# Kernel optimization log

Hardware: AMD Instinct MI355X
Metric: run time of the kernel (lower is better)

The kernel has to match this reference:

```python
import jax, jax.numpy as jnp
import numpy as np

S = 60            # voxel grid side
N = 100000        # active voxels
M_PAD = 60000     # padded pairs per kernel offset
C_IN = 64
C_OUT = 64
KV = 27           # kernel volume (3^3)
CENTER = 13


def _build_maps():
    rng = np.random.default_rng(0)
    lin = rng.choice(S ** 3, size=N, replace=False)
    coords = np.stack(np.unravel_index(lin, (S, S, S)), axis=1).astype(np.int64)  # [N,3]
    lut = -np.ones(S ** 3, dtype=np.int64)
    lut[lin] = np.arange(N)
    imap = -np.ones((KV - 1, M_PAD), dtype=np.int32)
    omap = -np.ones((KV - 1, M_PAD), dtype=np.int32)
    row = 0
    for k in range(KV):
        if k == CENTER:
            continue
        d = np.array([k // 9 - 1, (k // 3) % 3 - 1, k % 3 - 1])
        nb = coords + d
        valid = np.all((nb >= 0) & (nb < S), axis=1)
        linnb = nb[:, 0] * S * S + nb[:, 1] * S + nb[:, 2]
        j = np.where(valid, lut[np.clip(linnb, 0, S ** 3 - 1)], -1)
        mask = j >= 0
        src = np.nonzero(mask)[0].astype(np.int32)   # input idx (gather)
        dst = j[mask].astype(np.int32)               # output idx (scatter)
        m = min(src.shape[0], M_PAD)
        imap[row, :m] = src[:m]
        omap[row, :m] = dst[:m]
        row += 1
    return imap, omap


def setup_inputs() -> dict:
    key = jax.random.key(0)
    kf, kw = jax.random.split(key)
    feats = jax.random.normal(kf, (N, C_IN), dtype=jnp.float32)
    stdv = 1.0 / np.sqrt(C_OUT * KV)
    kernel = jax.random.uniform(kw, (KV, C_IN, C_OUT), dtype=jnp.float32,
                                minval=-stdv, maxval=stdv)
    imap_np, omap_np = _build_maps()
    return {
        "feats": feats,
        "kernel": kernel,
        "imap": jnp.asarray(imap_np),
        "omap": jnp.asarray(omap_np),
    }


def reference(feats, kernel, imap, omap):
    # Submanifold sparse 3D conv: center weight applied densely,
    # 26 neighbor offsets via gather -> per-offset GEMM -> scatter-add.
    # feats: [N, Cin], kernel: [27, Cin, Cout], imap/omap: [26, M] (-1 = pad)
    koff = jnp.concatenate([jnp.arange(CENTER), jnp.arange(CENTER + 1, KV)])
    w_off = kernel[koff]                                   # [26, Cin, Cout]
    out = feats @ kernel[CENTER]                           # [N, Cout] center GEMM
    valid = (imap >= 0)                                    # [26, M]
    gathered = feats[jnp.clip(imap, 0)] * valid[..., None].astype(feats.dtype)  # [26, M, Cin]
    partial = jnp.einsum('kmc,kco->kmo', gathered, w_off)  # [26, M, Cout]
    dst = jnp.where(valid, omap, 0).reshape(-1)            # padded rows contribute zeros
    out = out.at[dst].add(partial.reshape(-1, partial.shape[-1]))
    return out
```

## Files before the change

kernel.cpp:

```cpp
#include <hip/hip_runtime.h>


#define N_PTS 100000
#define MPAD  60000
#define C     64
#define NSL   27

typedef short bf16x8 __attribute__((ext_vector_type(8)));
typedef float f32x4  __attribute__((ext_vector_type(4)));

static __device__ inline unsigned short f2bf(float x) {
    unsigned int u = __float_as_uint(x);
    u += 0x7fffu + ((u >> 16) & 1u);
    return (unsigned short)(u >> 16);
}

#define FEATS16_BYTES ((size_t)(N_PTS + 1) * C * 2)
#define WFRAG_OFF     (((FEATS16_BYTES) + 255) & ~(size_t)255)
#define WFRAG_BYTES   ((size_t)NSL * 8192)
#define NBR_OFF       (WFRAG_OFF + WFRAG_BYTES)
#define NBR_BYTES     ((size_t)26 * N_PTS * 4)

#define FEAT_ITEMS 800008
#define WF_ITEMS   (NSL * 2 * 4 * 64)
#define SCAT_ITEMS (26 * MPAD / 4)
#define PREP_TOTAL (FEAT_ITEMS + WF_ITEMS + SCAT_ITEMS)

__global__ __launch_bounds__(256) void prep_one(const float* __restrict__ feats,
                                                const float* __restrict__ kern,
                                                const int* __restrict__ imap,
                                                const int* __restrict__ omap,
                                                unsigned short* __restrict__ f16,
                                                unsigned short* __restrict__ wf,
                                                int* __restrict__ nbr) {
    const int idx = blockIdx.x * 256 + threadIdx.x;
    if (idx < FEAT_ITEMS) {
        bf16x8* dst = (bf16x8*)f16;
        if (idx < FEAT_ITEMS - 8) {
            const float4* src = (const float4*)feats;
            const float4 a = src[2 * idx];
            const float4 b = src[2 * idx + 1];
            bf16x8 v;
            v[0] = (short)f2bf(a.x); v[1] = (short)f2bf(a.y);
            v[2] = (short)f2bf(a.z); v[3] = (short)f2bf(a.w);
            v[4] = (short)f2bf(b.x); v[5] = (short)f2bf(b.y);
            v[6] = (short)f2bf(b.z); v[7] = (short)f2bf(b.w);
            dst[idx] = v;
        } else {
            dst[idx] = (bf16x8){0, 0, 0, 0, 0, 0, 0, 0};
        }
    } else if (idx < FEAT_ITEMS + WF_ITEMS) {
        const int w = idx - FEAT_ITEMS;
        const int lane = w & 63;
        const int rest = w >> 6;
        const int ct = rest & 3;
        const int kk = (rest >> 2) & 1;
        const int s  = rest >> 3;
        bf16x8 v = (bf16x8){0, 0, 0, 0, 0, 0, 0, 0};
        if (s < NSL) {
            const int q = lane >> 4, t = lane & 15;
            const int ksrc = (s == 26) ? 13 : (s + (s >= 13 ? 1 : 0));
            const int k0 = kk * 32 + q * 8;
            const int n  = ct * 16 + t;
            const float* wp = kern + (size_t)ksrc * 4096 + n;
            #pragma unroll
            for (int j = 0; j < 8; ++j) v[j] = (short)f2bf(wp[(size_t)(k0 + j) * 64]);
        }
        ((bf16x8*)wf)[w] = v;
    } else {
        const int k = idx - (FEAT_ITEMS + WF_ITEMS);
        if (k < SCAT_ITEMS) {
            const int s = k / (MPAD / 4);
            const int v = k - s * (MPAD / 4);
            const int4 iv = ((const int4*)(imap + (size_t)s * MPAD))[v];
            const int4 ov = ((const int4*)(omap + (size_t)s * MPAD))[v];
            int* nb = nbr + (size_t)s * N_PTS;
            if (iv.x >= 0) nb[ov.x] = iv.x;
            if (iv.y >= 0) nb[ov.y] = iv.y;
            if (iv.z >= 0) nb[ov.z] = iv.z;
            if (iv.w >= 0) nb[ov.w] = iv.w;
        }
    }
}

__global__ __launch_bounds__(128, 3) void spconv_main(const unsigned short* __restrict__ f16,
                                                      const unsigned short* __restrict__ wf,
                                                      const int* __restrict__ nbr,
                                                      float* __restrict__ out) {
    const int lane = threadIdx.x & 63;
    const int wave = threadIdx.x >> 6;
    const int q = lane >> 4, t = lane & 15;
    const int R0 = blockIdx.x * 64 + wave * 32;
    const int row0 = R0 + t;
    const int row1 = R0 + 16 + t;
    const bool inb0 = (row0 < N_PTS);
    const bool inb1 = (row1 < N_PTS);
    const int safe0 = inb0 ? row0 : 0;
    const int safe1 = inb1 ? row1 : 0;

    const bf16x8* fv = (const bf16x8*)f16;
    const bf16x8* bv = (const bf16x8*)wf;

    int j0r[26], j1r[26];
    #pragma unroll
    for (int s = 0; s < 26; ++s) {
        j0r[s] = nbr[(size_t)s * N_PTS + safe0];
        j1r[s] = nbr[(size_t)s * N_PTS + safe1];
    }

    f32x4 acc[2][4];
    #pragma unroll
    for (int a = 0; a < 2; ++a)
        #pragma unroll
        for (int c = 0; c < 4; ++c)
            acc[a][c] = (f32x4){0.f, 0.f, 0.f, 0.f};

    #pragma unroll
    for (int s = 0; s < NSL; ++s) {
        int j0, j1;
        if (s == 26) {
            j0 = inb0 ? row0 : -1;
            j1 = inb1 ? row1 : -1;
        } else {
            j0 = inb0 ? j0r[s] : -1;
            j1 = inb1 ? j1r[s] : -1;
        }
        const int jz0 = ((unsigned)j0 < (unsigned)N_PTS) ? j0 : N_PTS;
        const int jz1 = ((unsigned)j1 < (unsigned)N_PTS) ? j1 : N_PTS;
        const bf16x8* a0p = fv + (size_t)jz0 * 8;
        const bf16x8* a1p = fv + (size_t)jz1 * 8;
        const bf16x8 A0 = a0p[q];
        const bf16x8 A1 = a0p[4 + q];
        const bf16x8 A2 = a1p[q];
        const bf16x8 A3 = a1p[4 + q];
        const bf16x8* bp = bv + (size_t)s * 512;
        bf16x8 B0[4], B1[4];
        #pragma unroll
        for (int ct = 0; ct < 4; ++ct) {
            B0[ct] = bp[ct * 64 + lane];
            B1[ct] = bp[256 + ct * 64 + lane];
        }
        #pragma unroll
        for (int ct = 0; ct < 4; ++ct) {
            acc[0][ct] = __builtin_amdgcn_mfma_f32_16x16x32_bf16(A0, B0[ct], acc[0][ct], 0, 0, 0);
            acc[1][ct] = __builtin_amdgcn_mfma_f32_16x16x32_bf16(A2, B0[ct], acc[1][ct], 0, 0, 0);
        }
        #pragma unroll
        for (int ct = 0; ct < 4; ++ct) {
            acc[0][ct] = __builtin_amdgcn_mfma_f32_16x16x32_bf16(A1, B1[ct], acc[0][ct], 0, 0, 0);
            acc[1][ct] = __builtin_amdgcn_mfma_f32_16x16x32_bf16(A3, B1[ct], acc[1][ct], 0, 0, 0);
        }
    }

    #pragma unroll
    for (int tile = 0; tile < 2; ++tile) {
        #pragma unroll
        for (int i = 0; i < 4; ++i) {
            const int r = R0 + tile * 16 + 4 * q + i;
            if (r < N_PTS) {
                #pragma unroll
                for (int ct = 0; ct < 4; ++ct)
                    out[(size_t)r * C + ct * 16 + t] = acc[tile][ct][i];
            }
        }
    }
}

extern "C" void kernel_launch(void* const* d_in, const int* in_sizes, int n_in,
                              void* d_out, int out_size, void* d_ws, size_t ws_size,
                              hipStream_t stream) {
    const float* feats = (const float*)d_in[0];
    const float* kern  = (const float*)d_in[1];
    const int*   imap  = (const int*)d_in[2];
    const int*   omap  = (const int*)d_in[3];

    char* ws = (char*)d_ws;
    unsigned short* f16 = (unsigned short*)ws;
    unsigned short* wfr = (unsigned short*)(ws + WFRAG_OFF);
    int*            nbr = (int*)(ws + NBR_OFF);

    prep_one<<<dim3((PREP_TOTAL + 255) / 256), dim3(256), 0, stream>>>(
        feats, kern, imap, omap, f16, wfr, nbr);
    spconv_main<<<dim3((N_PTS + 63) / 64), dim3(128), 0, stream>>>(
        f16, wfr, nbr, (float*)d_out);
}
```

Measured before the change: 158.4 us.

## Stage weights in LDS with triple-buffered async loads and software-pipelined gathers

Restructures the main kernel so each block of 4 waves (16 rows per wave) shares weight fragments staged into a triple-buffered LDS ring via global_load_lds. Neighbor-index loads and feature gathers are prefetched two slices ahead, with explicit vmcnt waits and barriers between slices. MFMA sections get raised priority. This is meant to cut redundant global weight reads and the register-heavy upfront index preload, and to overlap gather latency with compute. It adds a barrier per slice and relies on hand-counted vmcnt values being exactly right.

```diff
diff --git a/kernel.cpp b/kernel.cpp
--- a/kernel.cpp
+++ b/kernel.cpp
@@ -83,85 +83,104 @@
     }
 }
 
-__global__ __launch_bounds__(128, 3) void spconv_main(const unsigned short* __restrict__ f16,
+static __device__ inline void gl_lds(const char* g, char* l) {
+    __builtin_amdgcn_global_load_lds(
+        (const __attribute__((address_space(1))) unsigned int*)g,
+        (__attribute__((address_space(3))) unsigned int*)l, 16, 0, 0);
+}
+
+#define WAITV(n) asm volatile("s_waitcnt vmcnt(" #n ")" ::: "memory")
+#define FENCE    asm volatile("" ::: "memory")
+
+__global__ __launch_bounds__(256, 4) void spconv_main(const unsigned short* __restrict__ f16,
                                                       const unsigned short* __restrict__ wf,
                                                       const int* __restrict__ nbr,
                                                       float* __restrict__ out) {
+    __shared__ __align__(16) char bsm[3][8192];
+
     const int lane = threadIdx.x & 63;
     const int wave = threadIdx.x >> 6;
     const int q = lane >> 4, t = lane & 15;
-    const int R0 = blockIdx.x * 64 + wave * 32;
-    const int row0 = R0 + t;
-    const int row1 = R0 + 16 + t;
-    const bool inb0 = (row0 < N_PTS);
-    const bool inb1 = (row1 < N_PTS);
-    const int safe0 = inb0 ? row0 : 0;
-    const int safe1 = inb1 ? row1 : 0;
+    const int R0 = blockIdx.x * 64 + wave * 16;
+    const int row = R0 + t;
+    const bool inb = (row < N_PTS);
+    const int safe = inb ? row : 0;
 
     const bf16x8* fv = (const bf16x8*)f16;
-    const bf16x8* bv = (const bf16x8*)wf;
-
-    int j0r[26], j1r[26];
+    const char* wfb  = (const char*)wf;
+
+    int jr[3];
+    bf16x8 Ar[3][2];
+
+#define LOADJ(s_)  do { jr[(s_) % 3] = nbr[(size_t)(s_) * N_PTS + safe]; } while (0)
+
+#define GATHER(s_) do { \
+        int j_ = ((s_) == 26) ? (inb ? row : -1) : (inb ? jr[(s_) % 3] : -1); \
+        const int jz = ((unsigned)j_ < (unsigned)N_PTS) ? j_ : N_PTS; \
+        const bf16x8* ap = fv + (size_t)jz * 8; \
+        Ar[(s_) % 3][0] = ap[q]; \
+        Ar[(s_) % 3][1] = ap[4 + q]; \
+    } while (0)
+
+#define STAGEB(s_) do { \
+        const char* gs = wfb + (size_t)(s_) * 8192 + wave * 2048 + lane * 16; \
+        char* bd = (char*)bsm[(s_) % 3] + wave * 2048; \
+        gl_lds(gs, bd); gl_lds(gs + 1024, bd + 1024); \
+    } while (0)
+
+    LOADJ(0); LOADJ(1); FENCE;
+    STAGEB(0); FENCE; GATHER(0); FENCE; LOADJ(2); FENCE;
+    STAGEB(1); FENCE; GATHER(1); FENCE; LOADJ(3); FENCE;
+    WAITV(8);
+    __builtin_amdgcn_s_barrier();
+    FENCE;
+
+    f32x4 acc[4];
     #pragma unroll
-    for (int s = 0; s < 26; ++s) {
-        j0r[s] = nbr[(size_t)s * N_PTS + safe0];
-        j1r[s] = nbr[(size_t)s * N_PTS + safe1];
-    }
-
-    f32x4 acc[2][4];
-    #pragma unroll
-    for (int a = 0; a < 2; ++a)
-        #pragma unroll
-        for (int c = 0; c < 4; ++c)
-            acc[a][c] = (f32x4){0.f, 0.f, 0.f, 0.f};
+    for (int c = 0; c < 4; ++c) acc[c] = (f32x4){0.f, 0.f, 0.f, 0.f};
 
     #pragma unroll
     for (int s = 0; s < NSL; ++s) {
-        int j0, j1;
-        if (s == 26) {
-            j0 = inb0 ? row0 : -1;
-            j1 = inb1 ? row1 : -1;
-        } else {
-            j0 = inb0 ? j0r[s] : -1;
-            j1 = inb1 ? j1r[s] : -1;
-        }
-        const int jz0 = ((unsigned)j0 < (unsigned)N_PTS) ? j0 : N_PTS;
-        const int jz1 = ((unsigned)j1 < (unsigned)N_PTS) ? j1 : N_PTS;
-        const bf16x8* a0p = fv + (size_t)jz0 * 8;
-        const bf16x8* a1p = fv + (size_t)jz1 * 8;
-        const bf16x8 A0 = a0p[q];
-        const bf16x8 A1 = a0p[4 + q];
-        const bf16x8 A2 = a1p[q];
-        const bf16x8 A3 = a1p[4 + q];
-        const bf16x8* bp = bv + (size_t)s * 512;
+        if (s + 2 <= 26) { STAGEB(s + 2); FENCE; GATHER(s + 2); FENCE; }
+        if (s + 4 <= 25) { LOADJ(s + 4); FENCE; }
+
+        const char* bb = (const char*)bsm[s % 3];
         bf16x8 B0[4], B1[4];
         #pragma unroll
         for (int ct = 0; ct < 4; ++ct) {
-            B0[ct] = bp[ct * 64 + lane];
-            B1[ct] = bp[256 + ct * 64 + lane];
-        }
+            B0[ct] = *(const bf16x8*)(bb +        ct * 1024 + lane * 16);
+            B1[ct] = *(const bf16x8*)(bb + 4096 + ct * 1024 + lane * 16);
+        }
+        __builtin_amdgcn_s_setprio(1);
         #pragma unroll
-        for (int ct = 0; ct < 4; ++ct) {
-            acc[0][ct] = __builtin_amdgcn_mfma_f32_16x16x32_bf16(A0, B0[ct], acc[0][ct], 0, 0, 0);
-            acc[1][ct] = __builtin_amdgcn_mfma_f32_16x16x32_bf16(A2, B0[ct], acc[1][ct], 0, 0, 0);
-        }
+        for (int ct = 0; ct < 4; ++ct)
+            acc[ct] = __builtin_amdgcn_mfma_f32_16x16x32_bf16(Ar[s % 3][0], B0[ct], acc[ct], 0, 0, 0);
         #pragma unroll
-        for (int ct = 0; ct < 4; ++ct) {
-            acc[0][ct] = __builtin_amdgcn_mfma_f32_16x16x32_bf16(A1, B1[ct], acc[0][ct], 0, 0, 0);
-            acc[1][ct] = __builtin_amdgcn_mfma_f32_16x16x32_bf16(A3, B1[ct], acc[1][ct], 0, 0, 0);
+        for (int ct = 0; ct < 4; ++ct)
+            acc[ct] = __builtin_amdgcn_mfma_f32_16x16x32_bf16(Ar[s % 3][1], B1[ct], acc[ct], 0, 0, 0);
+        __builtin_amdgcn_s_setprio(0);
+
+        if (s < 26) {
+            if (s <= 21)      WAITV(8);
+            else if (s == 22) WAITV(7);
+            else if (s <= 24) WAITV(6);
+            else              WAITV(2);
+            __builtin_amdgcn_s_barrier();
+            FENCE;
         }
     }
 
+#undef LOADJ
+#undef GATHER
+#undef STAGEB
+
     #pragma unroll
-    for (int tile = 0; tile < 2; ++tile) {
-        #pragma unroll
-        for (int i = 0; i < 4; ++i) {
-            const int r = R0 + tile * 16 + 4 * q + i;
-            if (r < N_PTS) {
-                #pragma unroll
-                for (int ct = 0; ct < 4; ++ct)
-                    out[(size_t)r * C + ct * 16 + t] = acc[tile][ct][i];
-            }
+    for (int i = 0; i < 4; ++i) {
+        const int r = R0 + 4 * q + i;
+        if (r < N_PTS) {
+            #pragma unroll
+            for (int ct = 0; ct < 4; ++ct)
+                out[(size_t)r * C + ct * 16 + t] = acc[ct][i];
         }
     }
 }
@@ -181,6 +200,6 @@
 
     prep_one<<<dim3((PREP_TOTAL + 255) / 256), dim3(256), 0, stream>>>(
         feats, kern, imap, omap, f16, wfr, nbr);
-    spconv_main<<<dim3((N_PTS + 63) / 64), dim3(128), 0, stream>>>(
+    spconv_main<<<dim3((N_PTS + 63) / 64), dim3(256), 0, stream>>>(
         f16, wfr, nbr, (float*)d_out);
 }
```

After: 144.7 us. -8.6%, faster.
